# Performance work log

Measured on AMD Instinct MI355X. Metric: run time of the kernel, lower is better.

The kernel has to match this reference:

```python
import jax, jax.numpy as jnp
import numpy as np

N = 50000      # nodes
DEG = 32       # fixed out-degree used to build a synthetic CSR graph
E = N * DEG    # edges
F = 64         # in_feats = n_hidden = out_feats
K = 3          # n_kernels
DIM = 2        # pseudo-coordinate projection dim
L = 3          # n_layers + 1 GMMConv layers


def setup_inputs() -> dict:
    key = jax.random.key(0)
    ks = jax.random.split(key, 8)
    feat = jax.random.normal(ks[0], (N, F), jnp.float32)
    pseudo = jax.random.uniform(ks[1], (E, 2), jnp.float32)  # per-edge pseudo coords
    rowptr = jnp.arange(N + 1, dtype=jnp.int32) * DEG        # CSR row pointers
    colind = jax.random.randint(ks[2], (E,), 0, N, jnp.int32)  # neighbor (src) ids
    # Per-layer parameters, stacked over L layers (all layers are FxF here).
    proj_W = 0.5 * jax.random.normal(ks[3], (L, 2, DIM), jnp.float32)   # pseudo_proj Linear weight
    proj_b = jnp.zeros((L, DIM), jnp.float32)                            # pseudo_proj Linear bias
    fc_W = jax.random.normal(ks[4], (L, F, K * F), jnp.float32) / np.sqrt(F)  # GMMConv fc (no bias)
    mu = jax.random.normal(ks[5], (L, K, DIM), jnp.float32)              # Gaussian means
    inv_sigma = jnp.ones((L, K, DIM), jnp.float32)                       # inverse std-devs
    return {"feat": feat, "pseudo": pseudo, "rowptr": rowptr, "colind": colind,
            "proj_W": proj_W, "proj_b": proj_b, "fc_W": fc_W, "mu": mu,
            "inv_sigma": inv_sigma}


def reference(feat, pseudo, rowptr, colind, proj_W, proj_b, fc_W, mu, inv_sigma):
    n = feat.shape[0]
    e = colind.shape[0]
    n_layers = fc_W.shape[0]
    n_kern = mu.shape[1]
    # dst node of each edge from CSR rowptr (edge e belongs to row i iff rowptr[i] <= e < rowptr[i+1])
    dst = jnp.searchsorted(rowptr, jnp.arange(e, dtype=rowptr.dtype), side="right") - 1

    h = feat
    for i in range(n_layers):  # small fixed layer loop
        # pseudo_proj: Linear(2, dim) + Tanh, per edge -> [E, DIM]
        u = jnp.tanh(pseudo @ proj_W[i] + proj_b[i])
        # Gaussian kernel weights: w[e,k] = exp(-0.5 * sum_d ((u - mu)^2 * inv_sigma^2)) -> [E, K]
        diff = u[:, None, :] - mu[i][None, :, :]
        w = jnp.exp(-0.5 * jnp.sum(diff * diff * (inv_sigma[i][None, :, :] ** 2), axis=-1))
        out_dim = fc_W[i].shape[1] // n_kern
        hp = (h @ fc_W[i]).reshape(n, n_kern, out_dim)  # [N, K, out]
        # message per edge: sum_k w[e,k] * hp[src(e), k, :]; loop over small K to avoid [E,K,out]
        msg = jnp.zeros((e, out_dim), h.dtype)
        for k in range(n_kern):
            msg = msg + w[:, k:k + 1] * hp[colind, k, :]
        # scatter-reduce (sum aggregation) into destination nodes
        h = jax.ops.segment_sum(msg, dst, num_segments=n)
        # dropout is identity in eval mode (p=0.0)
    return h
```

## Files before the change

kernel.cpp:

```cpp
#include <hip/hip_runtime.h>
#include <math.h>

#define FEAT 64
#define NKERN 3

typedef __attribute__((ext_vector_type(8))) short short8;
typedef __attribute__((ext_vector_type(4))) float float4v;
typedef __attribute__((ext_vector_type(2))) float float2v;

__device__ __forceinline__ unsigned short f2bf(float f) {
    unsigned int u = __float_as_uint(f);
    u = (u + 0x7fffu + ((u >> 16) & 1u)) >> 16;
    return (unsigned short)u;
}
__device__ __forceinline__ float bf2f(unsigned short b) {
    return __uint_as_float(((unsigned int)b) << 16);
}
__device__ __forceinline__ float fast_tanh(float x) {
    float e = __expf(2.f * x);
    return fmaf(-2.f, __builtin_amdgcn_rcpf(e + 1.f), 1.f);
}

__global__ __launch_bounds__(256) void prep_kernel(
    const float* __restrict__ x, unsigned short* __restrict__ y, int n4,
    const float* __restrict__ fcW,
    unsigned short* __restrict__ Bth, unsigned short* __restrict__ Btl,
    int totalW, int nCastBlocks)
{
    int b = blockIdx.x;
    if (b < nCastBlocks) {
        int i = b * 256 + threadIdx.x;
        if (i >= n4) return;
        float4 v = ((const float4*)x)[i];
        ushort4 o;
        o.x = f2bf(v.x); o.y = f2bf(v.y); o.z = f2bf(v.z); o.w = f2bf(v.w);
        ((ushort4*)y)[i] = o;
    } else {
        int idx = (b - nCastBlocks) * 256 + threadIdx.x;
        if (idx >= totalW) return;
        int l   = idx / (FEAT * 192);
        int rem = idx - l * (FEAT * 192);
        int f   = rem / 192;
        int jp  = rem - f * 192;
        int k = jp >> 6, j = jp & 63;
        float v = fcW[(size_t)l * 12288 + j * 192 + k * 64 + f];
        unsigned short hi = f2bf(v);
        int dst = l * 12288 +
                  ((((f >> 4) * 6 + (jp >> 5)) * 4 + ((jp >> 3) & 3)) * 16 + (f & 15)) * 8 +
                  (jp & 7);
        Bth[dst] = hi;
        Btl[dst] = f2bf(v - bf2f(hi));
    }
}

__global__ __launch_bounds__(256, 4) void layer_kernel(
    const unsigned short* __restrict__ h,
    const int*   __restrict__ rowptr,
    const int*   __restrict__ colind,
    const float* __restrict__ pseudo,
    const float* __restrict__ projW,
    const float* __restrict__ projB,
    const float* __restrict__ mu,
    const float* __restrict__ isg,
    int layer,
    const unsigned short* __restrict__ Bth,
    const unsigned short* __restrict__ Btl,
    float* __restrict__ out,
    unsigned short* __restrict__ hnext,
    int n_nodes, int last_layer)
{
    __shared__ __align__(16) unsigned short Atile[3264];
    __shared__ __align__(16) unsigned int   Wlds[4][4][132];
    int tid  = threadIdx.x;
    int wv   = tid >> 6;
    int lane = tid & 63;
    int t0   = blockIdx.x * 16;

    const float* pw = projW + layer * 4;
    const float* pb = projB + layer * 2;
    const float* mm = mu  + layer * 6;
    const float* ss = isg + layer * 6;
    float pw0 = pw[0], pw1 = pw[1], pw2 = pw[2], pw3 = pw[3];
    float pb0 = pb[0], pb1 = pb[1];
    float m0 = mm[0], m1 = mm[1], m2 = mm[2], m3 = mm[3], m4 = mm[4], m5 = mm[5];
    float c0 = -0.5f * ss[0] * ss[0], c1 = -0.5f * ss[1] * ss[1];
    float c2 = -0.5f * ss[2] * ss[2], c3 = -0.5f * ss[3] * ss[3];
    float c4 = -0.5f * ss[4] * ss[4], c5 = -0.5f * ss[5] * ss[5];

    int half = lane >> 5;
    int p    = lane & 31;
    const char* hb = (const char*)h;

    bool fastp[2];
    #pragma unroll
    for (int tt = 0; tt < 2; ++tt) {
        int node = t0 + wv * 4 + tt * 2 + half;
        int ncl  = node < n_nodes - 1 ? node : (n_nodes - 1);
        int rp   = rowptr[ncl];
        int deg  = rowptr[ncl + 1] - rp;
        bool fast = __all((deg == 32) && (node < n_nodes));
        fastp[tt] = fast;
        if (fast) {
            int ei = rp + p;
            int cc = colind[ei];
            float2 ps = ((const float2*)pseudo)[ei];
            float u0 = fast_tanh(fmaf(ps.x, pw0, fmaf(ps.y, pw2, pb0)));
            float u1 = fast_tanh(fmaf(ps.x, pw1, fmaf(ps.y, pw3, pb1)));
            float d0 = u0 - m0, d1 = u1 - m1;
            float w0v = __expf(fmaf(d0 * d0, c0, d1 * d1 * c1));
            d0 = u0 - m2; d1 = u1 - m3;
            float w1v = __expf(fmaf(d0 * d0, c2, d1 * d1 * c3));
            d0 = u0 - m4; d1 = u1 - m5;
            float w2v = __expf(fmaf(d0 * d0, c4, d1 * d1 * c5));
            uint4 recw;
            recw.x = ((unsigned int)cc) << 7;
            recw.y = __float_as_uint(w0v);
            recw.z = __float_as_uint(w1v);
            recw.w = __float_as_uint(w2v);
            *(uint4*)&Wlds[wv][tt * 2 + half][p * 4] = recw;
        }
    }

    if (fastp[0] && fastp[1]) {
        int g  = lane >> 4;
        int p4 = lane & 15;
        unsigned int fo4 = (unsigned int)(p4 * 8);
        const unsigned int* Wg = &Wlds[wv][g][0];

        float2v a0l = {0.f,0.f}, a0h = {0.f,0.f};
        float2v a1l = {0.f,0.f}, a1h = {0.f,0.f};
        float2v a2l = {0.f,0.f}, a2h = {0.f,0.f};

        uint4 r0 = *(const uint4*)(Wg + 0);
        uint4 r1 = *(const uint4*)(Wg + 4);
        uint4 r2 = *(const uint4*)(Wg + 8);
        uint4 r3 = *(const uint4*)(Wg + 12);

        #pragma unroll
        for (int b = 0; b < 8; ++b) {
            uint2 h0 = *(const uint2*)(hb + (r0.x + fo4));
            uint2 h1 = *(const uint2*)(hb + (r1.x + fo4));
            uint2 h2 = *(const uint2*)(hb + (r2.x + fo4));
            uint2 h3 = *(const uint2*)(hb + (r3.x + fo4));
            uint4 n0, n1, n2, n3;
            if (b < 7) {
                n0 = *(const uint4*)(Wg + (b + 1) * 16 + 0);
                n1 = *(const uint4*)(Wg + (b + 1) * 16 + 4);
                n2 = *(const uint4*)(Wg + (b + 1) * 16 + 8);
                n3 = *(const uint4*)(Wg + (b + 1) * 16 + 12);
            }
#define CONSUME(hv, rc) do {                                                   \
            float2v vlo, vhi;                                                  \
            vlo.x = __uint_as_float((hv).x << 16);                             \
            vlo.y = __uint_as_float((hv).x & 0xffff0000u);                     \
            vhi.x = __uint_as_float((hv).y << 16);                             \
            vhi.y = __uint_as_float((hv).y & 0xffff0000u);                     \
            float w0 = __uint_as_float((rc).y);                                \
            float w1 = __uint_as_float((rc).z);                                \
            float w2 = __uint_as_float((rc).w);                                \
            float2v s0 = {w0, w0}, s1 = {w1, w1}, s2 = {w2, w2};               \
            a0l = __builtin_elementwise_fma(vlo, s0, a0l);                     \
            a0h = __builtin_elementwise_fma(vhi, s0, a0h);                     \
            a1l = __builtin_elementwise_fma(vlo, s1, a1l);                     \
            a1h = __builtin_elementwise_fma(vhi, s1, a1h);                     \
            a2l = __builtin_elementwise_fma(vlo, s2, a2l);                     \
            a2h = __builtin_elementwise_fma(vhi, s2, a2h);                     \
        } while (0)
            CONSUME(h0, r0);
            CONSUME(h1, r1);
            CONSUME(h2, r2);
            CONSUME(h3, r3);
#undef CONSUME
            if (b < 7) { r0 = n0; r1 = n1; r2 = n2; r3 = n3; }
        }

        int m  = wv * 4 + g;
        int j0 = p4 * 4;
        int sa = (j0 >> 5) * 544 + ((j0 >> 3) & 3) * 136 + m * 8 + (j0 & 7);
        unsigned int k0l, k0h, k1l, k1h, k2l, k2h;
        asm("v_cvt_pk_bf16_f32 %0, %1, %2" : "=v"(k0l) : "v"(a0l.x), "v"(a0l.y));
        asm("v_cvt_pk_bf16_f32 %0, %1, %2" : "=v"(k0h) : "v"(a0h.x), "v"(a0h.y));
        asm("v_cvt_pk_bf16_f32 %0, %1, %2" : "=v"(k1l) : "v"(a1l.x), "v"(a1l.y));
        asm("v_cvt_pk_bf16_f32 %0, %1, %2" : "=v"(k1h) : "v"(a1h.x), "v"(a1h.y));
        asm("v_cvt_pk_bf16_f32 %0, %1, %2" : "=v"(k2l) : "v"(a2l.x), "v"(a2l.y));
        asm("v_cvt_pk_bf16_f32 %0, %1, %2" : "=v"(k2h) : "v"(a2h.x), "v"(a2h.y));
        uint2 w0 = {k0l, k0h}, w1 = {k1l, k1h}, w2 = {k2l, k2h};
        *(uint2*)&Atile[sa]        = w0;
        *(uint2*)&Atile[sa + 1088] = w1;
        *(uint2*)&Atile[sa + 2176] = w2;
    } else {
        for (int mq = 0; mq < 4; ++mq) {
            int node = t0 + wv * 4 + mq;
            float a0 = 0.f, a1 = 0.f, a2 = 0.f;
            if (node < n_nodes) {
                int nu = __builtin_amdgcn_readfirstlane(node);
                int r0 = rowptr[nu];
                int dg = rowptr[nu + 1] - r0;
                for (int i = 0; i < dg; ++i) {
                    int cc = colind[r0 + i];
                    float px = pseudo[(size_t)(r0 + i) * 2];
                    float py = pseudo[(size_t)(r0 + i) * 2 + 1];
                    float u0 = fast_tanh(fmaf(px, pw0, fmaf(py, pw2, pb0)));
                    float u1 = fast_tanh(fmaf(px, pw1, fmaf(py, pw3, pb1)));
                    float d0 = u0 - m0, d1 = u1 - m1;
                    float w0e = __expf(fmaf(d0 * d0, c0, d1 * d1 * c1));
                    d0 = u0 - m2; d1 = u1 - m3;
                    float w1e = __expf(fmaf(d0 * d0, c2, d1 * d1 * c3));
                    d0 = u0 - m4; d1 = u1 - m5;
                    float w2e = __expf(fmaf(d0 * d0, c4, d1 * d1 * c5));
                    float vf = bf2f(h[(size_t)cc * FEAT + lane]);
                    a0 = fmaf(w0e, vf, a0);
                    a1 = fmaf(w1e, vf, a1);
                    a2 = fmaf(w2e, vf, a2);
                }
            }
            int sb = (lane >> 5) * 544 + ((lane >> 3) & 3) * 136 + (wv * 4 + mq) * 8 + (lane & 7);
            Atile[sb]        = f2bf(a0);
            Atile[sb + 1088] = f2bf(a1);
            Atile[sb + 2176] = f2bf(a2);
        }
    }
    __syncthreads();

    int q  = lane >> 4;
    int nn = lane & 15;
    const unsigned short* bt0 = Bth + (((wv * 6) * 4 + q) * 16 + nn) * 8;
    const unsigned short* bt1 = Btl + (((wv * 6) * 4 + q) * 16 + nn) * 8;
    float4v acc = (float4v){0.f, 0.f, 0.f, 0.f};
    #pragma unroll
    for (int ks = 0; ks < 6; ++ks) {
        short8 ah = *(const short8*)&Atile[ks * 544 + q * 136 + nn * 8];
        short8 bh = *(const short8*)(bt0 + ks * 512);
        short8 bl = *(const short8*)(bt1 + ks * 512);
        acc = __builtin_amdgcn_mfma_f32_16x16x32_bf16(ah, bh, acc, 0, 0, 0);
        acc = __builtin_amdgcn_mfma_f32_16x16x32_bf16(ah, bl, acc, 0, 0, 0);
    }
    #pragma unroll
    for (int r = 0; r < 4; ++r) {
        int row = t0 + q * 4 + r;
        if (row < n_nodes) {
            if (last_layer)
                out[(size_t)row * 64 + wv * 16 + nn] = acc[r];
            else
                hnext[(size_t)row * 64 + wv * 16 + nn] = f2bf(acc[r]);
        }
    }
}

extern "C" void kernel_launch(void* const* d_in, const int* in_sizes, int n_in,
                              void* d_out, int out_size, void* d_ws, size_t ws_size,
                              hipStream_t stream)
{
    const float* feat   = (const float*)d_in[0];
    const float* pseudo = (const float*)d_in[1];
    const int*   rowptr = (const int*)d_in[2];
    const int*   colind = (const int*)d_in[3];
    const float* projW  = (const float*)d_in[4];
    const float* projB  = (const float*)d_in[5];
    const float* fcW    = (const float*)d_in[6];
    const float* mu     = (const float*)d_in[7];
    const float* isg    = (const float*)d_in[8];
    float* out = (float*)d_out;

    int n  = in_sizes[0] / FEAT;
    int n_layers = in_sizes[6] / (FEAT * NKERN * FEAT);

    unsigned short* hbA = (unsigned short*)d_ws;
    unsigned short* hbB = hbA + (size_t)n * FEAT;
    unsigned short* Bth = hbB + (size_t)n * FEAT;
    unsigned short* Btl = Bth + (size_t)n_layers * 12288;

    int n4 = n * FEAT / 4;
    int totalW = n_layers * FEAT * 192;
    int castBlocks = (n4 + 255) / 256;
    int wpBlocks   = (totalW + 255) / 256;

    dim3 blk(256);
    dim3 prepGrid(castBlocks + wpBlocks);
    dim3 layerGrid((n + 15) / 16);
    dim3 layerBlk(256);

    prep_kernel<<<prepGrid, blk, 0, stream>>>(
        feat, hbA, n4, fcW, Bth, Btl, totalW, castBlocks);

    const unsigned short* hin = hbA;
    for (int l = 0; l < n_layers; ++l) {
        int last = (l == n_layers - 1);
        unsigned short* hb_out = (l == 0) ? hbB : hbA;
        layer_kernel<<<layerGrid, layerBlk, 0, stream>>>(
            hin, rowptr, colind, pseudo, projW, projB, mu, isg, l,
            Bth + (size_t)l * 12288, Btl + (size_t)l * 12288,
            out, hb_out, n, last);
        hin = hb_out;
    }
}
```

Baseline: 167.0 us.

## Double block to 512 threads and split each node's edges across half-waves

Raises the layer kernel block size to 512 threads, so each wave handles 2 nodes instead of 4. Each node's 32 edges are split between two 16-lane groups, and the partial sums are combined with xor-16 shuffles. The intent is more memory-level parallelism in the gather phase and shorter per-thread serial loops. In exchange, the hand-written software prefetch of LDS edge records is dropped, the shuffle reduction adds work, and only half the waves do the MFMA stage.

```diff
diff --git a/kernel.cpp b/kernel.cpp
--- a/kernel.cpp
+++ b/kernel.cpp
@@ -19,6 +19,9 @@
 __device__ __forceinline__ float fast_tanh(float x) {
     float e = __expf(2.f * x);
     return fmaf(-2.f, __builtin_amdgcn_rcpf(e + 1.f), 1.f);
+}
+__device__ __forceinline__ float sxor16(float v) {
+    return __shfl_xor(v, 16, 64);
 }
 
 __global__ __launch_bounds__(256) void prep_kernel(
@@ -53,7 +56,7 @@
     }
 }
 
-__global__ __launch_bounds__(256, 4) void layer_kernel(
+__global__ __launch_bounds__(512, 8) void layer_kernel(
     const unsigned short* __restrict__ h,
     const int*   __restrict__ rowptr,
     const int*   __restrict__ colind,
@@ -70,7 +73,7 @@
     int n_nodes, int last_layer)
 {
     __shared__ __align__(16) unsigned short Atile[3264];
-    __shared__ __align__(16) unsigned int   Wlds[4][4][132];
+    __shared__ __align__(16) unsigned int   Wlds[8][2][132];
     int tid  = threadIdx.x;
     int wv   = tid >> 6;
     int lane = tid & 63;
@@ -91,109 +94,90 @@
     int p    = lane & 31;
     const char* hb = (const char*)h;
 
-    bool fastp[2];
-    #pragma unroll
-    for (int tt = 0; tt < 2; ++tt) {
-        int node = t0 + wv * 4 + tt * 2 + half;
-        int ncl  = node < n_nodes - 1 ? node : (n_nodes - 1);
-        int rp   = rowptr[ncl];
-        int deg  = rowptr[ncl + 1] - rp;
-        bool fast = __all((deg == 32) && (node < n_nodes));
-        fastp[tt] = fast;
-        if (fast) {
-            int ei = rp + p;
-            int cc = colind[ei];
-            float2 ps = ((const float2*)pseudo)[ei];
-            float u0 = fast_tanh(fmaf(ps.x, pw0, fmaf(ps.y, pw2, pb0)));
-            float u1 = fast_tanh(fmaf(ps.x, pw1, fmaf(ps.y, pw3, pb1)));
-            float d0 = u0 - m0, d1 = u1 - m1;
-            float w0v = __expf(fmaf(d0 * d0, c0, d1 * d1 * c1));
-            d0 = u0 - m2; d1 = u1 - m3;
-            float w1v = __expf(fmaf(d0 * d0, c2, d1 * d1 * c3));
-            d0 = u0 - m4; d1 = u1 - m5;
-            float w2v = __expf(fmaf(d0 * d0, c4, d1 * d1 * c5));
-            uint4 recw;
-            recw.x = ((unsigned int)cc) << 7;
-            recw.y = __float_as_uint(w0v);
-            recw.z = __float_as_uint(w1v);
-            recw.w = __float_as_uint(w2v);
-            *(uint4*)&Wlds[wv][tt * 2 + half][p * 4] = recw;
-        }
-    }
-
-    if (fastp[0] && fastp[1]) {
-        int g  = lane >> 4;
-        int p4 = lane & 15;
-        unsigned int fo4 = (unsigned int)(p4 * 8);
-        const unsigned int* Wg = &Wlds[wv][g][0];
+    int node = t0 + wv * 2 + half;
+    int ncl  = node < n_nodes - 1 ? node : (n_nodes - 1);
+    int rp   = rowptr[ncl];
+    int deg  = rowptr[ncl + 1] - rp;
+    bool fast = __all((deg == 32) && (node < n_nodes));
+    if (fast) {
+        int ei = rp + p;
+        int cc = colind[ei];
+        float2 ps = ((const float2*)pseudo)[ei];
+        float u0 = fast_tanh(fmaf(ps.x, pw0, fmaf(ps.y, pw2, pb0)));
+        float u1 = fast_tanh(fmaf(ps.x, pw1, fmaf(ps.y, pw3, pb1)));
+        float d0 = u0 - m0, d1 = u1 - m1;
+        float w0v = __expf(fmaf(d0 * d0, c0, d1 * d1 * c1));
+        d0 = u0 - m2; d1 = u1 - m3;
+        float w1v = __expf(fmaf(d0 * d0, c2, d1 * d1 * c3));
+        d0 = u0 - m4; d1 = u1 - m5;
+        float w2v = __expf(fmaf(d0 * d0, c4, d1 * d1 * c5));
+        uint4 recw;
+        recw.x = ((unsigned int)cc) << 7;
+        recw.y = __float_as_uint(w0v);
+        recw.z = __float_as_uint(w1v);
+        recw.w = __float_as_uint(w2v);
+        *(uint4*)&Wlds[wv][half][p * 4] = recw;
+
+        int sub = (lane >> 4) & 1;
+        int ch  = lane & 15;
+        unsigned int fo = (unsigned int)(ch * 8);
+        const unsigned int* Wg = &Wlds[wv][half][0];
 
         float2v a0l = {0.f,0.f}, a0h = {0.f,0.f};
         float2v a1l = {0.f,0.f}, a1h = {0.f,0.f};
         float2v a2l = {0.f,0.f}, a2h = {0.f,0.f};
 
-        uint4 r0 = *(const uint4*)(Wg + 0);
-        uint4 r1 = *(const uint4*)(Wg + 4);
-        uint4 r2 = *(const uint4*)(Wg + 8);
-        uint4 r3 = *(const uint4*)(Wg + 12);
-
         #pragma unroll
-        for (int b = 0; b < 8; ++b) {
-            uint2 h0 = *(const uint2*)(hb + (r0.x + fo4));
-            uint2 h1 = *(const uint2*)(hb + (r1.x + fo4));
-            uint2 h2 = *(const uint2*)(hb + (r2.x + fo4));
-            uint2 h3 = *(const uint2*)(hb + (r3.x + fo4));
-            uint4 n0, n1, n2, n3;
-            if (b < 7) {
-                n0 = *(const uint4*)(Wg + (b + 1) * 16 + 0);
-                n1 = *(const uint4*)(Wg + (b + 1) * 16 + 4);
-                n2 = *(const uint4*)(Wg + (b + 1) * 16 + 8);
-                n3 = *(const uint4*)(Wg + (b + 1) * 16 + 12);
-            }
-#define CONSUME(hv, rc) do {                                                   \
-            float2v vlo, vhi;                                                  \
-            vlo.x = __uint_as_float((hv).x << 16);                             \
-            vlo.y = __uint_as_float((hv).x & 0xffff0000u);                     \
-            vhi.x = __uint_as_float((hv).y << 16);                             \
-            vhi.y = __uint_as_float((hv).y & 0xffff0000u);                     \
-            float w0 = __uint_as_float((rc).y);                                \
-            float w1 = __uint_as_float((rc).z);                                \
-            float w2 = __uint_as_float((rc).w);                                \
-            float2v s0 = {w0, w0}, s1 = {w1, w1}, s2 = {w2, w2};               \
-            a0l = __builtin_elementwise_fma(vlo, s0, a0l);                     \
-            a0h = __builtin_elementwise_fma(vhi, s0, a0h);                     \
-            a1l = __builtin_elementwise_fma(vlo, s1, a1l);                     \
-            a1h = __builtin_elementwise_fma(vhi, s1, a1h);                     \
-            a2l = __builtin_elementwise_fma(vlo, s2, a2l);                     \
-            a2h = __builtin_elementwise_fma(vhi, s2, a2h);                     \
-        } while (0)
-            CONSUME(h0, r0);
-            CONSUME(h1, r1);
-            CONSUME(h2, r2);
-            CONSUME(h3, r3);
-#undef CONSUME
-            if (b < 7) { r0 = n0; r1 = n1; r2 = n2; r3 = n3; }
-        }
-
-        int m  = wv * 4 + g;
-        int j0 = p4 * 4;
-        int sa = (j0 >> 5) * 544 + ((j0 >> 3) & 3) * 136 + m * 8 + (j0 & 7);
-        unsigned int k0l, k0h, k1l, k1h, k2l, k2h;
-        asm("v_cvt_pk_bf16_f32 %0, %1, %2" : "=v"(k0l) : "v"(a0l.x), "v"(a0l.y));
-        asm("v_cvt_pk_bf16_f32 %0, %1, %2" : "=v"(k0h) : "v"(a0h.x), "v"(a0h.y));
-        asm("v_cvt_pk_bf16_f32 %0, %1, %2" : "=v"(k1l) : "v"(a1l.x), "v"(a1l.y));
-        asm("v_cvt_pk_bf16_f32 %0, %1, %2" : "=v"(k1h) : "v"(a1h.x), "v"(a1h.y));
-        asm("v_cvt_pk_bf16_f32 %0, %1, %2" : "=v"(k2l) : "v"(a2l.x), "v"(a2l.y));
-        asm("v_cvt_pk_bf16_f32 %0, %1, %2" : "=v"(k2h) : "v"(a2h.x), "v"(a2h.y));
-        uint2 w0 = {k0l, k0h}, w1 = {k1l, k1h}, w2 = {k2l, k2h};
-        *(uint2*)&Atile[sa]        = w0;
-        *(uint2*)&Atile[sa + 1088] = w1;
-        *(uint2*)&Atile[sa + 2176] = w2;
+        for (int i = 0; i < 16; ++i) {
+            int e = sub * 16 + i;
+            uint4 rc = *(const uint4*)(Wg + e * 4);
+            uint2 hv = *(const uint2*)(hb + (rc.x + fo));
+            float2v vlo, vhi;
+            vlo.x = __uint_as_float(hv.x << 16);
+            vlo.y = __uint_as_float(hv.x & 0xffff0000u);
+            vhi.x = __uint_as_float(hv.y << 16);
+            vhi.y = __uint_as_float(hv.y & 0xffff0000u);
+            float w0 = __uint_as_float(rc.y);
+            float w1 = __uint_as_float(rc.z);
+            float w2 = __uint_as_float(rc.w);
+            float2v s0 = {w0, w0}, s1 = {w1, w1}, s2 = {w2, w2};
+            a0l = __builtin_elementwise_fma(vlo, s0, a0l);
+            a0h = __builtin_elementwise_fma(vhi, s0, a0h);
+            a1l = __builtin_elementwise_fma(vlo, s1, a1l);
+            a1h = __builtin_elementwise_fma(vhi, s1, a1h);
+            a2l = __builtin_elementwise_fma(vlo, s2, a2l);
+            a2h = __builtin_elementwise_fma(vhi, s2, a2h);
+        }
+
+        a0l.x += sxor16(a0l.x); a0l.y += sxor16(a0l.y);
+        a0h.x += sxor16(a0h.x); a0h.y += sxor16(a0h.y);
+        a1l.x += sxor16(a1l.x); a1l.y += sxor16(a1l.y);
+        a1h.x += sxor16(a1h.x); a1h.y += sxor16(a1h.y);
+        a2l.x += sxor16(a2l.x); a2l.y += sxor16(a2l.y);
+        a2h.x += sxor16(a2h.x); a2h.y += sxor16(a2h.y);
+
+        if (sub == 0) {
+            int m  = wv * 2 + half;
+            int j0 = ch * 4;
+            int sa = (j0 >> 5) * 544 + ((j0 >> 3) & 3) * 136 + m * 8 + (j0 & 7);
+            unsigned int k0l, k0h, k1l, k1h, k2l, k2h;
+            asm("v_cvt_pk_bf16_f32 %0, %1, %2" : "=v"(k0l) : "v"(a0l.x), "v"(a0l.y));
+            asm("v_cvt_pk_bf16_f32 %0, %1, %2" : "=v"(k0h) : "v"(a0h.x), "v"(a0h.y));
+            asm("v_cvt_pk_bf16_f32 %0, %1, %2" : "=v"(k1l) : "v"(a1l.x), "v"(a1l.y));
+            asm("v_cvt_pk_bf16_f32 %0, %1, %2" : "=v"(k1h) : "v"(a1h.x), "v"(a1h.y));
+            asm("v_cvt_pk_bf16_f32 %0, %1, %2" : "=v"(k2l) : "v"(a2l.x), "v"(a2l.y));
+            asm("v_cvt_pk_bf16_f32 %0, %1, %2" : "=v"(k2h) : "v"(a2h.x), "v"(a2h.y));
+            uint2 w0 = {k0l, k0h}, w1 = {k1l, k1h}, w2 = {k2l, k2h};
+            *(uint2*)&Atile[sa]        = w0;
+            *(uint2*)&Atile[sa + 1088] = w1;
+            *(uint2*)&Atile[sa + 2176] = w2;
+        }
     } else {
-        for (int mq = 0; mq < 4; ++mq) {
-            int node = t0 + wv * 4 + mq;
+        for (int mq = 0; mq < 2; ++mq) {
+            int node2 = t0 + wv * 2 + mq;
             float a0 = 0.f, a1 = 0.f, a2 = 0.f;
-            if (node < n_nodes) {
-                int nu = __builtin_amdgcn_readfirstlane(node);
+            if (node2 < n_nodes) {
+                int nu = __builtin_amdgcn_readfirstlane(node2);
                 int r0 = rowptr[nu];
                 int dg = rowptr[nu + 1] - r0;
                 for (int i = 0; i < dg; ++i) {
@@ -214,7 +198,7 @@
                     a2 = fmaf(w2e, vf, a2);
                 }
             }
-            int sb = (lane >> 5) * 544 + ((lane >> 3) & 3) * 136 + (wv * 4 + mq) * 8 + (lane & 7);
+            int sb = (lane >> 5) * 544 + ((lane >> 3) & 3) * 136 + (wv * 2 + mq) * 8 + (lane & 7);
             Atile[sb]        = f2bf(a0);
             Atile[sb + 1088] = f2bf(a1);
             Atile[sb + 2176] = f2bf(a2);
@@ -222,27 +206,29 @@
     }
     __syncthreads();
 
-    int q  = lane >> 4;
-    int nn = lane & 15;
-    const unsigned short* bt0 = Bth + (((wv * 6) * 4 + q) * 16 + nn) * 8;
-    const unsigned short* bt1 = Btl + (((wv * 6) * 4 + q) * 16 + nn) * 8;
-    float4v acc = (float4v){0.f, 0.f, 0.f, 0.f};
-    #pragma unroll
-    for (int ks = 0; ks < 6; ++ks) {
-        short8 ah = *(const short8*)&Atile[ks * 544 + q * 136 + nn * 8];
-        short8 bh = *(const short8*)(bt0 + ks * 512);
-        short8 bl = *(const short8*)(bt1 + ks * 512);
-        acc = __builtin_amdgcn_mfma_f32_16x16x32_bf16(ah, bh, acc, 0, 0, 0);
-        acc = __builtin_amdgcn_mfma_f32_16x16x32_bf16(ah, bl, acc, 0, 0, 0);
-    }
-    #pragma unroll
-    for (int r = 0; r < 4; ++r) {
-        int row = t0 + q * 4 + r;
-        if (row < n_nodes) {
-            if (last_layer)
-                out[(size_t)row * 64 + wv * 16 + nn] = acc[r];
-            else
-                hnext[(size_t)row * 64 + wv * 16 + nn] = f2bf(acc[r]);
+    if (wv < 4) {
+        int q  = lane >> 4;
+        int nn = lane & 15;
+        const unsigned short* bt0 = Bth + (((wv * 6) * 4 + q) * 16 + nn) * 8;
+        const unsigned short* bt1 = Btl + (((wv * 6) * 4 + q) * 16 + nn) * 8;
+        float4v acc = (float4v){0.f, 0.f, 0.f, 0.f};
+        #pragma unroll
+        for (int ks = 0; ks < 6; ++ks) {
+            short8 ah = *(const short8*)&Atile[ks * 544 + q * 136 + nn * 8];
+            short8 bh = *(const short8*)(bt0 + ks * 512);
+            short8 bl = *(const short8*)(bt1 + ks * 512);
+            acc = __builtin_amdgcn_mfma_f32_16x16x32_bf16(ah, bh, acc, 0, 0, 0);
+            acc = __builtin_amdgcn_mfma_f32_16x16x32_bf16(ah, bl, acc, 0, 0, 0);
+        }
+        #pragma unroll
+        for (int r = 0; r < 4; ++r) {
+            int row = t0 + q * 4 + r;
+            if (row < n_nodes) {
+                if (last_layer)
+                    out[(size_t)row * 64 + wv * 16 + nn] = acc[r];
+                else
+                    hnext[(size_t)row * 64 + wv * 16 + nn] = f2bf(acc[r]);
+            }
         }
     }
 }
@@ -278,7 +264,7 @@
     dim3 blk(256);
     dim3 prepGrid(castBlocks + wpBlocks);
     dim3 layerGrid((n + 15) / 16);
-    dim3 layerBlk(256);
+    dim3 layerBlk(512);
 
     prep_kernel<<<prepGrid, blk, 0, stream>>>(
         feat, hbA, n4, fcW, Bth, Btl, totalW, castBlocks);
```

Measured after the change: 172.2 us. 3.1% more time.
